# Kernel tuning notes

Measured on AMD Instinct MI355X. Metric: run time of the kernel, lower is better.

Reference implementation:

```python
import jax, jax.numpy as jnp
import numpy as np

N_LEVELS = 16  # 3**16 = 43_046_721


def setup_inputs() -> dict:
    key = jax.random.key(0)
    k1, k2 = jax.random.split(key)
    f = jax.random.normal(k1, (3 ** N_LEVELS,), dtype=jnp.float32)
    # torch.rand -> uniform [0, 1)
    Phi_P = jax.random.uniform(k2, (N_LEVELS, 3, 3), dtype=jnp.float32)
    return {"f": f, "Phi_P": Phi_P}


def reference(f, Phi_P):
    N = Phi_P.shape[0]
    # Row-orthonormalize each 3x3 block: QR of Phi_P^T, then take Q^T
    Q, _ = jnp.linalg.qr(jnp.swapaxes(Phi_P, -2, -1))  # batched reduced QR
    Phi = jnp.swapaxes(Q, -2, -1)  # [N, 3, 3], orthonormal rows

    # Recursive Haar-style butterfly. At level i, f has length 3**(N-i).
    # Detail coefficients (rows j=1,2) land in slots [3**(N-i-1), 3**(N-i));
    # the row-0 (average) branch recurses. Build segments and concatenate
    # in reverse to avoid scatter into a preallocated buffer.
    segs = []
    for i in range(N):
        fm = f.reshape(-1, 3)            # [3**(N-i-1), 3]
        d1 = fm @ Phi[i, 1, :]           # detail j=1
        d2 = fm @ Phi[i, 2, :]           # detail j=2
        segs.append(jnp.concatenate([d1, d2]))
        f = fm @ Phi[i, 0, :]            # average branch, length /3
    # f now has length 1; its single entry is f_hat[0]
    f_hat = jnp.concatenate([f[:1]] + segs[::-1])
    return f_hat
```

## Files before the change

kernel.cpp:

```cpp
#include <hip/hip_runtime.h>

#define TPB 256

typedef float f32x4 __attribute__((ext_vector_type(4)));

__device__ __forceinline__ void block_sync_lds() {
    asm volatile("s_waitcnt lgkmcnt(0)" ::: "memory");
    __builtin_amdgcn_s_barrier();
    asm volatile("" ::: "memory");
}

__device__ __forceinline__ float sgpr(float x) {
    return __int_as_float(__builtin_amdgcn_readfirstlane(__float_as_int(x)));
}

__device__ __forceinline__ void qr3(const float* __restrict__ M, float* __restrict__ P) {
    float A[3][3];
#pragma unroll
    for (int r = 0; r < 3; ++r)
#pragma unroll
        for (int c = 0; c < 3; ++c)
            A[r][c] = M[c * 3 + r];

    float V[3][3], tau[3];
#pragma unroll
    for (int k = 0; k < 3; ++k) {
        float alpha = A[k][k];
        float xn2 = 0.f;
#pragma unroll
        for (int r = k + 1; r < 3; ++r) xn2 += A[r][k] * A[r][k];
        float t = 0.f;
        float v[3] = {0.f, 0.f, 0.f};
        v[k] = 1.f;
        if (xn2 > 0.f) {
            float beta = -copysignf(sqrtf(alpha * alpha + xn2), alpha);
            t = (beta - alpha) / beta;
            float inv = 1.f / (alpha - beta);
#pragma unroll
            for (int r = k + 1; r < 3; ++r) v[r] = A[r][k] * inv;
#pragma unroll
            for (int c = 0; c < 3; ++c) {
                if (c < k) continue;
                float w = 0.f;
#pragma unroll
                for (int r = 0; r < 3; ++r) if (r >= k) w += v[r] * A[r][c];
                w *= t;
#pragma unroll
                for (int r = 0; r < 3; ++r) if (r >= k) A[r][c] -= w * v[r];
            }
        }
        tau[k] = t;
#pragma unroll
        for (int r = 0; r < 3; ++r) V[k][r] = v[r];
    }
    float Q[3][3] = {{1.f, 0.f, 0.f}, {0.f, 1.f, 0.f}, {0.f, 0.f, 1.f}};
#pragma unroll
    for (int k = 2; k >= 0; --k) {
#pragma unroll
        for (int c = 0; c < 3; ++c) {
            float w = 0.f;
#pragma unroll
            for (int r = 0; r < 3; ++r) w += V[k][r] * Q[r][c];
            w *= tau[k];
#pragma unroll
            for (int r = 0; r < 3; ++r) Q[r][c] -= w * V[k][r];
        }
    }
#pragma unroll
    for (int r = 0; r < 3; ++r)
#pragma unroll
        for (int c = 0; c < 3; ++c)
            P[r * 3 + c] = Q[c][r];
}

#define ORG_D1L0 0
#define ORG_D2L0 2312
#define ORG_D1L1 4624
#define ORG_D2L1 5400
#define ORG_D1L2 6176
#define ORG_D2L2 6440

__global__ __launch_bounds__(TPB) void fused3_kernel(
        const float* __restrict__ in, float* __restrict__ out,
        float* __restrict__ avg_out, const float* __restrict__ PhiP,
        int lvl, int m2) {
    __shared__ float s[6912];
    const int  t = threadIdx.x;
    const long b = blockIdx.x;
    const long nF = 27L * m2;
    const long fBase = 6912L * b;
    const long M0 = 9L * m2, M1 = 3L * m2, M2 = m2;

    const bool full = (256L * (b + 1) <= (long)m2);

    const long A0 = M0 + 2304L * b;
    const long A1 = 2 * M0 + 2304L * b;
    const long A2 = M1 + 768L * b;
    const long A3 = 2 * M1 + 768L * b;
    const long A4 = M2 + 256L * b;
    const long A5 = 2 * M2 + 256L * b;
    const int o0 = (int)(A0 & 3), o1 = (int)(A1 & 3), o2 = (int)(A2 & 3);
    const int o3 = (int)(A3 & 3), o4 = (int)(A4 & 3), o5 = (int)(A5 & 3);

    f32x4 v[7];
    if (full) {
        const f32x4* p4 = reinterpret_cast<const f32x4*>(in + fBase);
#pragma unroll
        for (int r = 0; r < 6; ++r) v[r] = p4[256 * r + t];
        if (t < 192) v[6] = p4[1536 + t];
    }

    float P[27];
    qr3(PhiP + 9L * lvl,       P + 0);
    qr3(PhiP + 9L * (lvl + 1), P + 9);
    qr3(PhiP + 9L * (lvl + 2), P + 18);
#pragma unroll
    for (int j = 0; j < 27; ++j) P[j] = sgpr(P[j]);

    if (full) {
#pragma unroll
        for (int r = 0; r < 6; ++r)
            *reinterpret_cast<f32x4*>(&s[4 * (256 * r + t)]) = v[r];
        if (t < 192)
            *reinterpret_cast<f32x4*>(&s[4 * (1536 + t)]) = v[6];
    } else {
        const long rem = nF - fBase;
        for (int i = t; i < 6912; i += TPB) s[i] = (i < rem) ? in[fBase + i] : 0.f;
    }
    block_sync_lds();

    float f[27];
#pragma unroll
    for (int j = 0; j < 27; ++j) f[j] = s[27 * t + j];
    block_sync_lds();

    float a[9];
#pragma unroll
    for (int g = 0; g < 9; ++g) {
        float x = f[3 * g], y = f[3 * g + 1], z = f[3 * g + 2];
        a[g] = x * P[0] + y * P[1] + z * P[2];
        s[ORG_D1L0 + o0 + 9 * t + g] = x * P[3] + y * P[4] + z * P[5];
        s[ORG_D2L0 + o1 + 9 * t + g] = x * P[6] + y * P[7] + z * P[8];
    }
    float bb[3];
#pragma unroll
    for (int h = 0; h < 3; ++h) {
        float x = a[3 * h], y = a[3 * h + 1], z = a[3 * h + 2];
        bb[h] = x * P[9] + y * P[10] + z * P[11];
        s[ORG_D1L1 + o2 + 3 * t + h] = x * P[12] + y * P[13] + z * P[14];
        s[ORG_D2L1 + o3 + 3 * t + h] = x * P[15] + y * P[16] + z * P[17];
    }
    float c;
    {
        float x = bb[0], y = bb[1], z = bb[2];
        c = x * P[18] + y * P[19] + z * P[20];
        s[ORG_D1L2 + o4 + t] = x * P[21] + y * P[22] + z * P[23];
        s[ORG_D2L2 + o5 + t] = x * P[24] + y * P[25] + z * P[26];
    }
    block_sync_lds();

#define STORE_SEC(ORG, A, O, CNT, ROUNDS)                                      \
    {                                                                          \
        float* dst = out + (A);                                                \
        const int aH = (4 - (O)) & 3;                                          \
        const int nb = ((CNT) - aH) >> 2;                                      \
        const int tl = (CNT) - aH - 4 * nb;                                    \
        if (t < aH) __builtin_nontemporal_store(s[(ORG) + (O) + t], dst + t);  \
        _Pragma("unroll")                                                      \
        for (int r = 0; r < (ROUNDS); ++r) {                                   \
            int idx = 256 * r + t;                                             \
            if (idx < nb) {                                                    \
                f32x4 vv = *reinterpret_cast<const f32x4*>(                    \
                    &s[(ORG) + (O) + aH + 4 * idx]);                           \
                __builtin_nontemporal_store(                                   \
                    vv, reinterpret_cast<f32x4*>(dst + aH) + idx);             \
            }                                                                  \
        }                                                                      \
        if (t < tl)                                                            \
            __builtin_nontemporal_store(s[(ORG) + (O) + aH + 4 * nb + t],      \
                                        dst + aH + 4 * nb + t);                \
    }

    if (full) {
        STORE_SEC(ORG_D1L0, A0, o0, 2304, 3);
        STORE_SEC(ORG_D2L0, A1, o1, 2304, 3);
        STORE_SEC(ORG_D1L1, A2, o2, 768, 1);
        STORE_SEC(ORG_D2L1, A3, o3, 768, 1);
        STORE_SEC(ORG_D1L2, A4, o4, 256, 1);
        STORE_SEC(ORG_D2L2, A5, o5, 256, 1);
        avg_out[256L * b + t] = c;
    } else {
#pragma unroll
        for (int r = 0; r < 9; ++r) {
            long i = 256 * r + t, g = 2304L * b + i;
            if (g < M0) {
                __builtin_nontemporal_store(s[ORG_D1L0 + o0 + i], out + M0 + g);
                __builtin_nontemporal_store(s[ORG_D2L0 + o1 + i], out + 2 * M0 + g);
            }
        }
#pragma unroll
        for (int r = 0; r < 3; ++r) {
            long i = 256 * r + t, g = 768L * b + i;
            if (g < M1) {
                __builtin_nontemporal_store(s[ORG_D1L1 + o2 + i], out + M1 + g);
                __builtin_nontemporal_store(s[ORG_D2L1 + o3 + i], out + 2 * M1 + g);
            }
        }
        long g = 256L * b + t;
        if (g < M2) {
            __builtin_nontemporal_store(s[ORG_D1L2 + o4 + t], out + M2 + g);
            __builtin_nontemporal_store(s[ORG_D2L2 + o5 + t], out + 2 * M2 + g);
            avg_out[g] = c;
        }
    }
#undef STORE_SEC
}

#define TTPB 1024
__global__ __launch_bounds__(TTPB) void tail_kernel(
        const float* __restrict__ in, float* __restrict__ out,
        const float* __restrict__ PhiP) {
    __shared__ float s0[2187];
    __shared__ float s1[729];
    __shared__ float sPhi[63];
    const int lt = threadIdx.x;

    for (int i = lt; i < 2187; i += TTPB) s0[i] = in[i];
    if (lt < 7) {
        float P[9];
        qr3(PhiP + 9L * (9 + lt), P);
#pragma unroll
        for (int j = 0; j < 9; ++j) sPhi[lt * 9 + j] = P[j];
    }
    __syncthreads();

    float* cur = s0;
    float* nxt = s1;
    int len = 2187;
#pragma unroll
    for (int L = 0; L < 7; ++L) {
        int m = len / 3;
        float p0 = sPhi[L * 9 + 0], p1 = sPhi[L * 9 + 1], p2 = sPhi[L * 9 + 2];
        float q0 = sPhi[L * 9 + 3], q1 = sPhi[L * 9 + 4], q2 = sPhi[L * 9 + 5];
        float r0 = sPhi[L * 9 + 6], r1 = sPhi[L * 9 + 7], r2 = sPhi[L * 9 + 8];
        for (int t = lt; t < m; t += TTPB) {
            float x = cur[3 * t], y = cur[3 * t + 1], z = cur[3 * t + 2];
            out[m + t]     = x * q0 + y * q1 + z * q2;
            out[2 * m + t] = x * r0 + y * r1 + z * r2;
            nxt[t]         = x * p0 + y * p1 + z * p2;
        }
        block_sync_lds();
        float* tmp = cur; cur = nxt; nxt = tmp;
        len = m;
    }
    if (lt == 0) out[0] = cur[0];
}

extern "C" void kernel_launch(void* const* d_in, const int* in_sizes, int n_in,
                              void* d_out, int out_size, void* d_ws, size_t ws_size,
                              hipStream_t stream) {
    const float* f    = (const float*)d_in[0];
    const float* PhiP = (const float*)d_in[1];
    float* out = (float*)d_out;
    float* ws  = (float*)d_ws;

    float* bufA = ws;
    float* bufB = bufA + 1594323;
    float* bufC = bufB + 59049;

    const int m2_0 = 1594323;
    fused3_kernel<<<(m2_0 + TPB - 1) / TPB, TPB, 0, stream>>>(f, out, bufA, PhiP, 0, m2_0);

    const int m2_1 = 59049;
    fused3_kernel<<<(m2_1 + TPB - 1) / TPB, TPB, 0, stream>>>(bufA, out, bufB, PhiP, 3, m2_1);

    const int m2_2 = 2187;
    fused3_kernel<<<(m2_2 + TPB - 1) / TPB, TPB, 0, stream>>>(bufB, out, bufC, PhiP, 6, m2_2);

    tail_kernel<<<1, TTPB, 0, stream>>>(bufC, out, PhiP);
}
```

Baseline: 85.02 us.

## Load input tiles directly into LDS and fold third fused pass into tail kernel

The main fused kernel now uses global_load_lds to move input tiles straight from global memory into shared memory, bypassing registers and removing the explicit register-to-LDS store. The third fused3 launch is removed, and the single-block tail kernel now handles levels 6 through 15, reading the 59049-element buffer from global memory. This saves one kernel launch and its inter-kernel gap. In exchange, roughly 20k elements are processed serially by one 1024-thread block, with larger LDS arrays.

```diff
diff --git a/kernel.cpp b/kernel.cpp
--- a/kernel.cpp
+++ b/kernel.cpp
@@ -12,6 +12,12 @@
 
 __device__ __forceinline__ float sgpr(float x) {
     return __int_as_float(__builtin_amdgcn_readfirstlane(__float_as_int(x)));
+}
+
+__device__ __forceinline__ void gload_lds16(const float* g, float* l) {
+    __builtin_amdgcn_global_load_lds(
+        (const __attribute__((address_space(1))) void*)g,
+        (__attribute__((address_space(3))) void*)l, 16, 0, 0);
 }
 
 __device__ __forceinline__ void qr3(const float* __restrict__ M, float* __restrict__ P) {
@@ -102,12 +108,20 @@
     const int o0 = (int)(A0 & 3), o1 = (int)(A1 & 3), o2 = (int)(A2 & 3);
     const int o3 = (int)(A3 & 3), o4 = (int)(A4 & 3), o5 = (int)(A5 & 3);
 
-    f32x4 v[7];
     if (full) {
-        const f32x4* p4 = reinterpret_cast<const f32x4*>(in + fBase);
-#pragma unroll
-        for (int r = 0; r < 6; ++r) v[r] = p4[256 * r + t];
-        if (t < 192) v[6] = p4[1536 + t];
+        const float* src = in + fBase;
+#pragma unroll
+        for (int r = 0; r < 6; ++r) {
+            int c = 256 * r + t;
+            gload_lds16(src + 4 * c, &s[4 * c]);
+        }
+        if (t < 192) {
+            int c = 1536 + t;
+            gload_lds16(src + 4 * c, &s[4 * c]);
+        }
+    } else {
+        const long rem = nF - fBase;
+        for (int i = t; i < 6912; i += TPB) s[i] = (i < rem) ? in[fBase + i] : 0.f;
     }
 
     float P[27];
@@ -117,17 +131,7 @@
 #pragma unroll
     for (int j = 0; j < 27; ++j) P[j] = sgpr(P[j]);
 
-    if (full) {
-#pragma unroll
-        for (int r = 0; r < 6; ++r)
-            *reinterpret_cast<f32x4*>(&s[4 * (256 * r + t)]) = v[r];
-        if (t < 192)
-            *reinterpret_cast<f32x4*>(&s[4 * (1536 + t)]) = v[6];
-    } else {
-        const long rem = nF - fBase;
-        for (int i = t; i < 6912; i += TPB) s[i] = (i < rem) ? in[fBase + i] : 0.f;
-    }
-    block_sync_lds();
+    __syncthreads();
 
     float f[27];
 #pragma unroll
@@ -220,34 +224,46 @@
 __global__ __launch_bounds__(TTPB) void tail_kernel(
         const float* __restrict__ in, float* __restrict__ out,
         const float* __restrict__ PhiP) {
-    __shared__ float s0[2187];
-    __shared__ float s1[729];
-    __shared__ float sPhi[63];
+    __shared__ float s0[19683];
+    __shared__ float s1[6561];
+    __shared__ float sPhi[90];
     const int lt = threadIdx.x;
 
-    for (int i = lt; i < 2187; i += TTPB) s0[i] = in[i];
-    if (lt < 7) {
+    if (lt < 10) {
         float P[9];
-        qr3(PhiP + 9L * (9 + lt), P);
+        qr3(PhiP + 9L * (6 + lt), P);
 #pragma unroll
         for (int j = 0; j < 9; ++j) sPhi[lt * 9 + j] = P[j];
     }
     __syncthreads();
+
+    {
+        float p0 = sPhi[0], p1 = sPhi[1], p2 = sPhi[2];
+        float q0 = sPhi[3], q1 = sPhi[4], q2 = sPhi[5];
+        float r0 = sPhi[6], r1 = sPhi[7], r2 = sPhi[8];
+        for (int u = lt; u < 19683; u += TTPB) {
+            float x = in[3 * u], y = in[3 * u + 1], z = in[3 * u + 2];
+            out[19683 + u]     = x * q0 + y * q1 + z * q2;
+            out[2 * 19683 + u] = x * r0 + y * r1 + z * r2;
+            s0[u]              = x * p0 + y * p1 + z * p2;
+        }
+    }
+    block_sync_lds();
 
     float* cur = s0;
     float* nxt = s1;
-    int len = 2187;
-#pragma unroll
-    for (int L = 0; L < 7; ++L) {
+    int len = 19683;
+#pragma unroll
+    for (int k = 1; k < 10; ++k) {
         int m = len / 3;
-        float p0 = sPhi[L * 9 + 0], p1 = sPhi[L * 9 + 1], p2 = sPhi[L * 9 + 2];
-        float q0 = sPhi[L * 9 + 3], q1 = sPhi[L * 9 + 4], q2 = sPhi[L * 9 + 5];
-        float r0 = sPhi[L * 9 + 6], r1 = sPhi[L * 9 + 7], r2 = sPhi[L * 9 + 8];
-        for (int t = lt; t < m; t += TTPB) {
-            float x = cur[3 * t], y = cur[3 * t + 1], z = cur[3 * t + 2];
-            out[m + t]     = x * q0 + y * q1 + z * q2;
-            out[2 * m + t] = x * r0 + y * r1 + z * r2;
-            nxt[t]         = x * p0 + y * p1 + z * p2;
+        float p0 = sPhi[k * 9 + 0], p1 = sPhi[k * 9 + 1], p2 = sPhi[k * 9 + 2];
+        float q0 = sPhi[k * 9 + 3], q1 = sPhi[k * 9 + 4], q2 = sPhi[k * 9 + 5];
+        float r0 = sPhi[k * 9 + 6], r1 = sPhi[k * 9 + 7], r2 = sPhi[k * 9 + 8];
+        for (int u = lt; u < m; u += TTPB) {
+            float x = cur[3 * u], y = cur[3 * u + 1], z = cur[3 * u + 2];
+            out[m + u]     = x * q0 + y * q1 + z * q2;
+            out[2 * m + u] = x * r0 + y * r1 + z * r2;
+            nxt[u]         = x * p0 + y * p1 + z * p2;
         }
         block_sync_lds();
         float* tmp = cur; cur = nxt; nxt = tmp;
@@ -266,7 +282,6 @@
 
     float* bufA = ws;
     float* bufB = bufA + 1594323;
-    float* bufC = bufB + 59049;
 
     const int m2_0 = 1594323;
     fused3_kernel<<<(m2_0 + TPB - 1) / TPB, TPB, 0, stream>>>(f, out, bufA, PhiP, 0, m2_0);
@@ -274,8 +289,5 @@
     const int m2_1 = 59049;
     fused3_kernel<<<(m2_1 + TPB - 1) / TPB, TPB, 0, stream>>>(bufA, out, bufB, PhiP, 3, m2_1);
 
-    const int m2_2 = 2187;
-    fused3_kernel<<<(m2_2 + TPB - 1) / TPB, TPB, 0, stream>>>(bufB, out, bufC, PhiP, 6, m2_2);
-
-    tail_kernel<<<1, TTPB, 0, stream>>>(bufC, out, PhiP);
-}
+    tail_kernel<<<1, TTPB, 0, stream>>>(bufB, out, PhiP);
+}
```

Result: no change. 83.81 us (-1.4%).

## Fuse middle six levels into one kernel and load tiles via direct global-to-LDS

Applied to the files above, without the earlier changes.

Replaces the second and third three-level fused launches with a single mid_kernel. Each of its 243 blocks processes 6561 inputs through six butterfly levels entirely in LDS, which removes one launch and one intermediate round trip through global memory. The first kernel's full-tile path now uses global_load_lds to move data directly into shared memory instead of staging it in registers. The new mid kernel runs the later levels with few active threads, so there is some serialization inside each block.

```diff
diff --git a/kernel.cpp b/kernel.cpp
--- a/kernel.cpp
+++ b/kernel.cpp
@@ -12,6 +12,17 @@
 
 __device__ __forceinline__ float sgpr(float x) {
     return __int_as_float(__builtin_amdgcn_readfirstlane(__float_as_int(x)));
+}
+
+__device__ __forceinline__ void gload_lds16(const float* g, float* l) {
+    __builtin_amdgcn_global_load_lds(
+        (const __attribute__((address_space(1))) void*)g,
+        (__attribute__((address_space(3))) void*)l, 16, 0, 0);
+}
+__device__ __forceinline__ void gload_lds4(const float* g, float* l) {
+    __builtin_amdgcn_global_load_lds(
+        (const __attribute__((address_space(1))) void*)g,
+        (__attribute__((address_space(3))) void*)l, 4, 0, 0);
 }
 
 __device__ __forceinline__ void qr3(const float* __restrict__ M, float* __restrict__ P) {
@@ -102,12 +113,20 @@
     const int o0 = (int)(A0 & 3), o1 = (int)(A1 & 3), o2 = (int)(A2 & 3);
     const int o3 = (int)(A3 & 3), o4 = (int)(A4 & 3), o5 = (int)(A5 & 3);
 
-    f32x4 v[7];
     if (full) {
-        const f32x4* p4 = reinterpret_cast<const f32x4*>(in + fBase);
-#pragma unroll
-        for (int r = 0; r < 6; ++r) v[r] = p4[256 * r + t];
-        if (t < 192) v[6] = p4[1536 + t];
+        const float* src = in + fBase;
+#pragma unroll
+        for (int r = 0; r < 6; ++r) {
+            int c = 256 * r + t;
+            gload_lds16(src + 4 * c, &s[4 * c]);
+        }
+        if (t < 192) {
+            int c = 1536 + t;
+            gload_lds16(src + 4 * c, &s[4 * c]);
+        }
+    } else {
+        const long rem = nF - fBase;
+        for (int i = t; i < 6912; i += TPB) s[i] = (i < rem) ? in[fBase + i] : 0.f;
     }
 
     float P[27];
@@ -117,17 +136,7 @@
 #pragma unroll
     for (int j = 0; j < 27; ++j) P[j] = sgpr(P[j]);
 
-    if (full) {
-#pragma unroll
-        for (int r = 0; r < 6; ++r)
-            *reinterpret_cast<f32x4*>(&s[4 * (256 * r + t)]) = v[r];
-        if (t < 192)
-            *reinterpret_cast<f32x4*>(&s[4 * (1536 + t)]) = v[6];
-    } else {
-        const long rem = nF - fBase;
-        for (int i = t; i < 6912; i += TPB) s[i] = (i < rem) ? in[fBase + i] : 0.f;
-    }
-    block_sync_lds();
+    __syncthreads();
 
     float f[27];
 #pragma unroll
@@ -216,6 +225,125 @@
 #undef STORE_SEC
 }
 
+__global__ __launch_bounds__(TPB) void mid_kernel(
+        const float* __restrict__ in, float* __restrict__ out,
+        float* __restrict__ avg_out, const float* __restrict__ PhiP) {
+    __shared__ float s[6912];
+    __shared__ float sc[243];
+    __shared__ float sc2[81];
+    __shared__ float sc3[27];
+    __shared__ float sPhi[54];
+    const int  t = threadIdx.x;
+    const long b = blockIdx.x;
+    const float* src = in + 6561L * b;
+
+#pragma unroll
+    for (int r = 0; r < 26; ++r) {
+        int i = 256 * r + t;
+        gload_lds4(src + i, &s[i]);
+    }
+    if (t < 6) {
+        float P[9];
+        qr3(PhiP + 9L * (3 + t), P);
+#pragma unroll
+        for (int j = 0; j < 9; ++j) sPhi[9 * t + j] = P[j];
+    }
+    __syncthreads();
+
+    float P[27];
+#pragma unroll
+    for (int j = 0; j < 27; ++j) P[j] = sgpr(sPhi[j]);
+
+    float f27[27];
+    const bool act = (t < 243);
+    if (act) {
+#pragma unroll
+        for (int j = 0; j < 27; ++j) f27[j] = s[27 * t + j];
+    }
+    block_sync_lds();
+
+    if (act) {
+        float a[9];
+#pragma unroll
+        for (int g = 0; g < 9; ++g) {
+            float x = f27[3 * g], y = f27[3 * g + 1], z = f27[3 * g + 2];
+            a[g] = x * P[0] + y * P[1] + z * P[2];
+            s[9 * t + g]        = x * P[3] + y * P[4] + z * P[5];
+            s[2187 + 9 * t + g] = x * P[6] + y * P[7] + z * P[8];
+        }
+        float bb[3];
+#pragma unroll
+        for (int h = 0; h < 3; ++h) {
+            float x = a[3 * h], y = a[3 * h + 1], z = a[3 * h + 2];
+            bb[h] = x * P[9] + y * P[10] + z * P[11];
+            s[4374 + 3 * t + h] = x * P[12] + y * P[13] + z * P[14];
+            s[5103 + 3 * t + h] = x * P[15] + y * P[16] + z * P[17];
+        }
+        float x = bb[0], y = bb[1], z = bb[2];
+        sc[t]        = x * P[18] + y * P[19] + z * P[20];
+        s[5832 + t]  = x * P[21] + y * P[22] + z * P[23];
+        s[6075 + t]  = x * P[24] + y * P[25] + z * P[26];
+    }
+    block_sync_lds();
+
+    if (t < 81) {
+        float x = sc[3 * t], y = sc[3 * t + 1], z = sc[3 * t + 2];
+        sc2[t]      = x * sPhi[27] + y * sPhi[28] + z * sPhi[29];
+        s[6318 + t] = x * sPhi[30] + y * sPhi[31] + z * sPhi[32];
+        s[6399 + t] = x * sPhi[33] + y * sPhi[34] + z * sPhi[35];
+    }
+    block_sync_lds();
+    if (t < 27) {
+        float x = sc2[3 * t], y = sc2[3 * t + 1], z = sc2[3 * t + 2];
+        sc3[t]      = x * sPhi[36] + y * sPhi[37] + z * sPhi[38];
+        s[6480 + t] = x * sPhi[39] + y * sPhi[40] + z * sPhi[41];
+        s[6507 + t] = x * sPhi[42] + y * sPhi[43] + z * sPhi[44];
+    }
+    block_sync_lds();
+    if (t < 9) {
+        float x = sc3[3 * t], y = sc3[3 * t + 1], z = sc3[3 * t + 2];
+        avg_out[9 * b + t] = x * sPhi[45] + y * sPhi[46] + z * sPhi[47];
+        s[6534 + t] = x * sPhi[48] + y * sPhi[49] + z * sPhi[50];
+        s[6543 + t] = x * sPhi[51] + y * sPhi[52] + z * sPhi[53];
+    }
+    block_sync_lds();
+
+    const long B0 = 2187L * b, B1 = 729L * b, B2 = 243L * b;
+    const long B3 = 81L * b, B4 = 27L * b, B5 = 9L * b;
+#pragma unroll
+    for (int r = 0; r < 9; ++r) {
+        int i = 256 * r + t;
+        if (i < 2187) {
+            __builtin_nontemporal_store(s[i],        out + 531441 + B0 + i);
+            __builtin_nontemporal_store(s[2187 + i], out + 2 * 531441 + B0 + i);
+        }
+    }
+#pragma unroll
+    for (int r = 0; r < 3; ++r) {
+        int i = 256 * r + t;
+        if (i < 729) {
+            __builtin_nontemporal_store(s[4374 + i], out + 177147 + B1 + i);
+            __builtin_nontemporal_store(s[5103 + i], out + 2 * 177147 + B1 + i);
+        }
+    }
+    if (t < 243) {
+        __builtin_nontemporal_store(s[5832 + t], out + 59049 + B2 + t);
+        __builtin_nontemporal_store(s[6075 + t], out + 2 * 59049 + B2 + t);
+    }
+    if (t < 81) {
+        __builtin_nontemporal_store(s[6318 + t], out + 19683 + B3 + t);
+        __builtin_nontemporal_store(s[6399 + t], out + 2 * 19683 + B3 + t);
+    }
+    if (t < 27) {
+        __builtin_nontemporal_store(s[6480 + t], out + 6561 + B4 + t);
+        __builtin_nontemporal_store(s[6507 + t], out + 2 * 6561 + B4 + t);
+    }
+    if (t < 9) {
+        __builtin_nontemporal_store(s[6534 + t], out + 2187 + B5 + t);
+        __builtin_nontemporal_store(s[6543 + t], out + 2 * 2187 + B5 + t);
+    }
+}
+
 #define TTPB 1024
 __global__ __launch_bounds__(TTPB) void tail_kernel(
         const float* __restrict__ in, float* __restrict__ out,
@@ -265,17 +393,12 @@
     float* ws  = (float*)d_ws;
 
     float* bufA = ws;
-    float* bufB = bufA + 1594323;
-    float* bufC = bufB + 59049;
+    float* bufC = bufA + 1594323;
 
     const int m2_0 = 1594323;
     fused3_kernel<<<(m2_0 + TPB - 1) / TPB, TPB, 0, stream>>>(f, out, bufA, PhiP, 0, m2_0);
 
-    const int m2_1 = 59049;
-    fused3_kernel<<<(m2_1 + TPB - 1) / TPB, TPB, 0, stream>>>(bufA, out, bufB, PhiP, 3, m2_1);
-
-    const int m2_2 = 2187;
-    fused3_kernel<<<(m2_2 + TPB - 1) / TPB, TPB, 0, stream>>>(bufB, out, bufC, PhiP, 6, m2_2);
+    mid_kernel<<<243, TPB, 0, stream>>>(bufA, out, bufC, PhiP);
 
     tail_kernel<<<1, TTPB, 0, stream>>>(bufC, out, PhiP);
 }
```

After: 72.39 us. -14.9%, faster.
